# Performance work log

Measured on AMD Instinct MI355X. Metric: run time of the kernel, lower is better.

The kernel has to match this reference:

```python
import jax, jax.numpy as jnp
import numpy as np

EPS = 1e-5

def _conv2d(x, w, b, pad):
    y = jax.lax.conv_general_dilated(x, w, (1, 1), [(pad, pad), (pad, pad)],
                                     dimension_numbers=('NCHW', 'OIHW', 'NCHW'))
    return y + b[None, :, None, None]

def _layernorm2d(x, g, beta):
    # channel-wise LayerNorm per spatial location (LayerNorm2d)
    mu = jnp.mean(x, axis=1, keepdims=True)
    var = jnp.var(x, axis=1, keepdims=True)
    return (x - mu) * jax.lax.rsqrt(var + EPS) * g[None, :, None, None] + beta[None, :, None, None]

def _deform_conv2d(x, offset, w, b, pad):
    # torchvision deform_conv2d semantics (stride 1, dilation 1, 1 group, no mask)
    # x: [B,C,H,W]; offset: [B,2*K*K,H,W] with (dy,dx) per kernel tap; w: [O,C,K,K]
    B, C, H, W = x.shape
    K = w.shape[-1]
    off = offset.reshape(B, K * K, 2, H, W)
    by = jnp.arange(H, dtype=x.dtype)[:, None]   # [H,1]
    bx = jnp.arange(W, dtype=x.dtype)[None, :]   # [1,W]

    def sample(im, py, px):
        # im [C,H,W], py/px [H,W] -> bilinear sample with zero padding outside
        y0 = jnp.floor(py); x0 = jnp.floor(px)
        wy = py - y0; wx = px - x0
        y0i = y0.astype(jnp.int32); x0i = x0.astype(jnp.int32)
        def g(yi, xi):
            valid = (yi >= 0) & (yi < H) & (xi >= 0) & (xi < W)
            v = im[:, jnp.clip(yi, 0, H - 1), jnp.clip(xi, 0, W - 1)]
            return v * valid.astype(im.dtype)
        v00 = g(y0i, x0i);     v01 = g(y0i, x0i + 1)
        v10 = g(y0i + 1, x0i); v11 = g(y0i + 1, x0i + 1)
        return (v00 * (1 - wy) * (1 - wx) + v01 * (1 - wy) * wx
                + v10 * wy * (1 - wx) + v11 * wy * wx)

    vsample = jax.vmap(sample)
    out = jnp.zeros((B, w.shape[0], H, W), dtype=x.dtype)
    for k in range(K * K):  # small fixed tap loop (<=49)
        ki, kj = k // K, k % K
        py = by + (ki - pad) + off[:, k, 0]  # [B,H,W]
        px = bx + (kj - pad) + off[:, k, 1]
        s = vsample(x, py, px)               # [B,C,H,W]
        out = out + jnp.einsum('bchw,oc->bohw', s, w[:, :, ki, kj])
    return out + b[None, :, None, None]


def setup_inputs() -> dict:
    key = jax.random.key(0)
    ks = jax.random.split(key, 12)
    B, C, H, W = 4, 64, 192, 192
    s = 0.02
    inp = {
        'x': jax.random.normal(ks[0], (B, C, H, W), jnp.float32),
        'ln_w': jnp.ones((C,), jnp.float32),
        'ln_b': jnp.zeros((C,), jnp.float32),
        'w_in': jax.random.normal(ks[1], (2 * C, C), jnp.float32) * s,
        'b_in': jnp.zeros((2 * C,), jnp.float32),
        'w_out': jax.random.normal(ks[2], (C, C), jnp.float32) * s,
        'b_out': jnp.zeros((C,), jnp.float32),
        'dw1': jax.random.normal(ks[3], (C, C, 7, 7), jnp.float32) * s,
        'db1': jnp.zeros((C,), jnp.float32),
        'dw2': jax.random.normal(ks[4], (C, C, 5, 5), jnp.float32) * s,
        'db2': jnp.zeros((C,), jnp.float32),
        'dw3': jax.random.normal(ks[5], (C, C, 3, 3), jnp.float32) * s,
        'db3': jnp.zeros((C,), jnp.float32),
        'ow1': jax.random.normal(ks[6], (2 * 7 * 7, C, 5, 5), jnp.float32) * s,
        'ob1': jnp.zeros((2 * 7 * 7,), jnp.float32),
        'ow2': jax.random.normal(ks[7], (2 * 5 * 5, C, 5, 5), jnp.float32) * s,
        'ob2': jnp.zeros((2 * 5 * 5,), jnp.float32),
        'ow3': jax.random.normal(ks[8], (2 * 3 * 3, C, 3, 3), jnp.float32) * s,
        'ob3': jnp.zeros((2 * 3 * 3,), jnp.float32),
    }
    return inp


def reference(x, ln_w, ln_b, w_in, b_in, w_out, b_out,
              dw1, db1, dw2, db2, dw3, db3,
              ow1, ob1, ow2, ob2, ow3, ob3):
    tmp = x
    h = _layernorm2d(x, ln_w, ln_b)
    h = jnp.einsum('bchw,oc->bohw', h, w_in) + b_in[None, :, None, None]  # 1x1 conv_in
    C = x.shape[1]
    x1, x2 = h[:, :C], h[:, C:]
    off = _conv2d(x1, ow1, ob1, 2)
    x1 = _deform_conv2d(x1, off, dw1, db1, 3)
    off = _conv2d(x1, ow2, ob2, 2)
    x1 = _deform_conv2d(x1, off, dw2, db2, 2)
    off = _conv2d(x1, ow3, ob3, 1)
    x1 = _deform_conv2d(x1, off, dw3, db3, 1)
    h = x1 + x2
    h = jnp.einsum('bchw,oc->bohw', h, w_out) + b_out[None, :, None, None]  # 1x1 conv_out
    return h + tmp
```

## Files before the change

kernel.cpp:

```cpp
#include <hip/hip_runtime.h>

#define HH 192
#define WID 192
#define HW (HH*WID)
#define CB 64
#define BB 4
#define NPOS (BB*HW)

typedef __attribute__((ext_vector_type(8))) _Float16 half8v;
typedef __attribute__((ext_vector_type(4))) _Float16 half4v;
typedef __attribute__((ext_vector_type(2))) _Float16 half2v;
typedef __attribute__((ext_vector_type(4))) float f32x4;
typedef __attribute__((ext_vector_type(16))) float f32x16;

static __device__ inline half8v splat8(_Float16 x) {
    half8v v = {x, x, x, x, x, x, x, x};
    return v;
}


template<int KK, int CO, int OP>
__global__ void k_wth(const float* __restrict__ w, _Float16* __restrict__ wt)
{
    int idx = blockIdx.x * 256 + threadIdx.x;
    constexpr int TOT = KK * OP * 64;
    if (idx >= TOT) return;
    int k  = idx / (OP * 64);
    int r  = idx % (OP * 64);
    int cs = r / (OP * 8);
    int r2 = r % (OP * 8);
    int o  = r2 / 8;
    int j  = r2 % 8;
    int c  = cs * 8 + j;
    float v = (o < CO) ? w[((size_t)o * 64 + c) * KK + k] : 0.f;
    wt[idx] = (_Float16)v;
}

__global__ __launch_bounds__(256) void k_lnconv_mfma(
    const float* __restrict__ x, const float* __restrict__ g, const float* __restrict__ be,
    const _Float16* __restrict__ wt_in, const float* __restrict__ b_in,
    _Float16* __restrict__ x1, _Float16* __restrict__ x2)
{
    int p0  = blockIdx.x * 128;
    int b   = p0 / HW;
    int hwb = p0 % HW;

    int lane = threadIdx.x & 63;
    int wave = threadIdx.x >> 6;
    int l31  = lane & 31;
    int h    = lane >> 5;
    int pos  = hwb + wave * 32 + l31;

    const float* xp = x + (size_t)b * CB * HW + pos;

    float v[32];
    float sum = 0.f, sumsq = 0.f;
#pragma unroll
    for (int m = 0; m < 4; m++)
#pragma unroll
        for (int j = 0; j < 8; j++) {
            float t = xp[(size_t)(m * 16 + h * 8 + j) * HW];
            v[m * 8 + j] = t; sum += t; sumsq += t * t;
        }
    sum   += __shfl_xor(sum, 32);
    sumsq += __shfl_xor(sumsq, 32);
    float mu  = sum * (1.f / 64.f);
    float var = sumsq * (1.f / 64.f) - mu * mu;
    float inv = rsqrtf(var + 1e-5f);

    half8v bf[4];
#pragma unroll
    for (int m = 0; m < 4; m++)
#pragma unroll
        for (int j = 0; j < 8; j++) {
            int c = m * 16 + h * 8 + j;
            bf[m][j] = (_Float16)((v[m * 8 + j] - mu) * inv * g[c] + be[c]);
        }

    f32x16 acc[4];
#pragma unroll
    for (int tI = 0; tI < 4; tI++)
#pragma unroll
        for (int r = 0; r < 16; r++) acc[tI][r] = 0.f;

    const half8v* wbase = (const half8v*)wt_in;
#pragma unroll
    for (int m = 0; m < 4; m++) {
        int cs = m * 2 + h;
        const half8v* wp = wbase + (size_t)cs * 128;
#pragma unroll
        for (int tI = 0; tI < 4; tI++) {
            half8v a = wp[tI * 32 + l31];
            acc[tI] = __builtin_amdgcn_mfma_f32_32x32x16_f16(a, bf[m], acc[tI], 0, 0, 0);
        }
    }

    _Float16* o1 = x1 + (size_t)b * HW * 64 + (size_t)pos * 8;
    _Float16* o2 = x2 + (size_t)b * HW * 64 + (size_t)pos * 8;
#pragma unroll
    for (int tI = 0; tI < 4; tI++) {
        _Float16* ob = (tI < 2) ? o1 : o2;
        int obase = (tI & 1) * 32;
#pragma unroll
        for (int gidx = 0; gidx < 4; gidx++) {
            int o = obase + gidx * 8 + 4 * h;
            float4 bb = *(const float4*)&b_in[tI * 32 + gidx * 8 + 4 * h];
            half4v r;
            r[0] = (_Float16)(acc[tI][gidx * 4 + 0] + bb.x);
            r[1] = (_Float16)(acc[tI][gidx * 4 + 1] + bb.y);
            r[2] = (_Float16)(acc[tI][gidx * 4 + 2] + bb.z);
            r[3] = (_Float16)(acc[tI][gidx * 4 + 3] + bb.w);
            *(half4v*)&ob[(size_t)(o >> 3) * HW * 8 + (o & 7)] = r;
        }
    }
}

template<int KD, int PAD, int HALO, int KO, int PADO, int CT>
__global__ __launch_bounds__(256) void k_fconv(
    const _Float16* __restrict__ xin,
    const _Float16* __restrict__ wto, const float* __restrict__ obias,
    const _Float16* __restrict__ wtd, const float* __restrict__ dbias,
    _Float16* __restrict__ outp)
{
    constexpr int KKD = KD * KD;
    constexpr int KKO = KO * KO;
    constexpr int RB = 16 + 2 * HALO;
    constexpr int WB = 8  + 2 * HALO;
    constexpr int OP = CT * 32;

    __shared__ half8v sm[RB * WB * 8];
    __shared__ unsigned int offs[KKD * 128];

    int bi  = blockIdx.x;
    int b   = bi / 288;
    int tt  = bi % 288;
    int by0 = (tt / 24) * 16;
    int bx0 = (tt % 24) * 8;
    int ry0 = by0 - HALO;
    int rx0 = bx0 - HALO;

    const _Float16* xb = xin + (size_t)b * HW * 64;

    {
        _Float16* smlin = (_Float16*)sm;
        constexpr int CH = RB * WB * 8;
        for (int i0 = 0; i0 < CH; i0 += 256) {
            int i    = i0 + (int)threadIdx.x;
            int wbse = i0 + ((int)threadIdx.x & 192);
            if (i < CH) {
                int pix = i >> 3;
                int ts  = i & 7;
                int pl  = ts ^ (pix & 7);
                int r   = pix / WB;
                int cc  = pix - r * WB;
                int yr  = ry0 + r;
                int xc  = rx0 + cc;
                bool ok = (yr >= 0 && yr < HH && xc >= 0 && xc < WID);
                if (ok) {
                    const _Float16* src = xb + ((size_t)pl * HW + (size_t)(yr * WID + xc)) * 8;
                    __builtin_amdgcn_global_load_lds(src, &smlin[(size_t)wbse * 8], 16, 0, 0);
                } else {
                    *(half8v*)&smlin[(size_t)i * 8] = splat8((_Float16)0.f);
                }
            }
        }
    }
    __syncthreads();

    int lane = threadIdx.x & 63;
    int wave = threadIdx.x >> 6;
    int l31  = lane & 31;
    int h    = lane >> 5;
    int prow = l31 >> 3;
    int pcol = l31 & 7;
    int xt   = bx0 + pcol;

    {
        int ct = wave % CT;
        int pp = wave / CT;

        int ytA[CT], pA[CT];
#pragma unroll
        for (int q = 0; q < CT; q++) {
            int g = pp * CT + q;
            ytA[q] = by0 + g * 4 + prow;
            pA[q]  = g * 32 + l31;
        }

        const half8v* wbase = (const half8v*)wto;

        f32x16 accO[CT];
#pragma unroll
        for (int q = 0; q < CT; q++)
#pragma unroll
            for (int r = 0; r < 16; r++) accO[q][r] = 0.f;

        int ki = 0, kj = 0;
        for (int k = 0; k < KKO; k++) {
            int ccx = (xt + kj - PADO) - rx0;
            int pixA[CT];
#pragma unroll
            for (int q = 0; q < CT; q++)
                pixA[q] = ((ytA[q] + ki - PADO) - ry0) * WB + ccx;

#pragma unroll
            for (int m = 0; m < 4; m++) {
                int cs = m * 2 + h;
                const half8v* wp = wbase + ((size_t)k * 8 + cs) * OP;
                half8v a = wp[ct * 32 + l31];
#pragma unroll
                for (int q = 0; q < CT; q++) {
                    half8v bf = sm[pixA[q] * 8 + (cs ^ (pixA[q] & 7))];
                    accO[q] = __builtin_amdgcn_mfma_f32_32x32x16_f16(a, bf, accO[q], 0, 0, 0);
                }
            }

            kj++;
            if (kj == KO) { kj = 0; ki++; }
        }

#pragma unroll
        for (int q = 0; q < CT; q++) {
#pragma unroll
            for (int gi = 0; gi < 4; gi++) {
                int obase = ct * 32 + 8 * gi + 4 * h;
#pragma unroll
                for (int pr = 0; pr < 2; pr++) {
                    int o  = obase + 2 * pr;
                    int kt = o >> 1;
                    if (kt < KKD) {
                        half2v hv;
                        hv[0] = (_Float16)(accO[q][gi * 4 + 2 * pr]     + obias[o]);
                        hv[1] = (_Float16)(accO[q][gi * 4 + 2 * pr + 1] + obias[o + 1]);
                        *(half2v*)&offs[kt * 128 + pA[q]] = hv;
                    }
                }
            }
        }
    }
    __syncthreads();

    int yt   = by0 + wave * 4 + prow;
    int p128 = wave * 32 + l31;

    const half8v* wbase = (const half8v*)wtd;

    f32x16 acc0 = {0.f,0.f,0.f,0.f,0.f,0.f,0.f,0.f,0.f,0.f,0.f,0.f,0.f,0.f,0.f,0.f};
    f32x16 acc1 = {0.f,0.f,0.f,0.f,0.f,0.f,0.f,0.f,0.f,0.f,0.f,0.f,0.f,0.f,0.f,0.f};

    int ki = 0, kj = 0;
    for (int k = 0; k < KKD; k++) {
        half2v ov = *(const half2v*)&offs[k * 128 + p128];
        float ox = (float)ov[0];
        float oy = (float)ov[1];

        half8v a0[4], a1[4];
#pragma unroll
        for (int m = 0; m < 4; m++) {
            int cs = m * 2 + h;
            const half8v* wp = wbase + ((size_t)k * 8 + cs) * 64;
            a0[m] = wp[l31];
            a1[m] = wp[32 + l31];
        }

        float py = (float)(yt + ki - PAD) + ox;
        float px = (float)(xt + kj - PAD) + oy;
        float fy = floorf(py), fx = floorf(px);
        float wy = py - fy, wx = px - fx;
        int iy0 = (int)fy, ix0 = (int)fx;
        int iy1 = iy0 + 1, ix1 = ix0 + 1;
        float m00 = (iy0 >= 0 && iy0 < HH && ix0 >= 0 && ix0 < WID) ? 1.f : 0.f;
        float m01 = (iy0 >= 0 && iy0 < HH && ix1 >= 0 && ix1 < WID) ? 1.f : 0.f;
        float m10 = (iy1 >= 0 && iy1 < HH && ix0 >= 0 && ix0 < WID) ? 1.f : 0.f;
        float m11 = (iy1 >= 0 && iy1 < HH && ix1 >= 0 && ix1 < WID) ? 1.f : 0.f;
        half8v w00v = splat8((_Float16)((1.f - wy) * (1.f - wx) * m00));
        half8v w01v = splat8((_Float16)((1.f - wy) * wx * m01));
        half8v w10v = splat8((_Float16)(wy * (1.f - wx) * m10));
        half8v w11v = splat8((_Float16)(wy * wx * m11));

        bool fast = (iy0 >= ry0) && (iy1 <= ry0 + RB - 1) &&
                    (ix0 >= rx0) && (ix1 <= rx0 + WB - 1);

        if (__builtin_expect(fast, 1)) {
            int p00 = (iy0 - ry0) * WB + (ix0 - rx0);
            int p01 = p00 + 1, p10 = p00 + WB, p11 = p00 + WB + 1;
            int s00 = p00 & 7, s01 = p01 & 7, s10 = p10 & 7, s11 = p11 & 7;
#pragma unroll
            for (int m = 0; m < 4; m++) {
                int cs = m * 2 + h;
                half8v c00 = sm[p00 * 8 + (cs ^ s00)];
                half8v c01 = sm[p01 * 8 + (cs ^ s01)];
                half8v c10 = sm[p10 * 8 + (cs ^ s10)];
                half8v c11 = sm[p11 * 8 + (cs ^ s11)];
                half8v bf = c00 * w00v + c01 * w01v + c10 * w10v + c11 * w11v;
                acc0 = __builtin_amdgcn_mfma_f32_32x32x16_f16(a0[m], bf, acc0, 0, 0, 0);
                acc1 = __builtin_amdgcn_mfma_f32_32x32x16_f16(a1[m], bf, acc1, 0, 0, 0);
            }
        } else {
            int cy0 = min(max(iy0, 0), HH - 1), cy1 = min(max(iy1, 0), HH - 1);
            int cx0 = min(max(ix0, 0), WID - 1), cx1 = min(max(ix1, 0), WID - 1);
            size_t i00 = (size_t)(cy0 * WID + cx0) * 8, i01 = (size_t)(cy0 * WID + cx1) * 8;
            size_t i10 = (size_t)(cy1 * WID + cx0) * 8, i11 = (size_t)(cy1 * WID + cx1) * 8;
#pragma unroll
            for (int m = 0; m < 4; m++) {
                const _Float16* xq = xb + (size_t)(m * 2 + h) * HW * 8;
                half8v c00 = *(const half8v*)(xq + i00);
                half8v c01 = *(const half8v*)(xq + i01);
                half8v c10 = *(const half8v*)(xq + i10);
                half8v c11 = *(const half8v*)(xq + i11);
                half8v bf = c00 * w00v + c01 * w01v + c10 * w10v + c11 * w11v;
                acc0 = __builtin_amdgcn_mfma_f32_32x32x16_f16(a0[m], bf, acc0, 0, 0, 0);
                acc1 = __builtin_amdgcn_mfma_f32_32x32x16_f16(a1[m], bf, acc1, 0, 0, 0);
            }
        }

        kj++;
        if (kj == KD) { kj = 0; ki++; }
    }

    int hwp = yt * WID + xt;
    _Float16* ob = outp + (size_t)b * HW * 64 + (size_t)hwp * 8 + 4 * h;
#pragma unroll
    for (int g = 0; g < 4; g++) {
        float4 bb0 = *(const float4*)&dbias[g * 8 + 4 * h];
        half4v r0;
        r0[0] = (_Float16)(acc0[g * 4 + 0] + bb0.x);
        r0[1] = (_Float16)(acc0[g * 4 + 1] + bb0.y);
        r0[2] = (_Float16)(acc0[g * 4 + 2] + bb0.z);
        r0[3] = (_Float16)(acc0[g * 4 + 3] + bb0.w);
        *(half4v*)&ob[(size_t)g * HW * 8] = r0;
        float4 bb1 = *(const float4*)&dbias[32 + g * 8 + 4 * h];
        half4v r1;
        r1[0] = (_Float16)(acc1[g * 4 + 0] + bb1.x);
        r1[1] = (_Float16)(acc1[g * 4 + 1] + bb1.y);
        r1[2] = (_Float16)(acc1[g * 4 + 2] + bb1.z);
        r1[3] = (_Float16)(acc1[g * 4 + 3] + bb1.w);
        *(half4v*)&ob[(size_t)(4 + g) * HW * 8] = r1;
    }
}

__global__ __launch_bounds__(256) void k_merge_mfma(
    const _Float16* __restrict__ x1f, const _Float16* __restrict__ x2,
    const float* __restrict__ xin, const _Float16* __restrict__ wt_out,
    const float* __restrict__ b_out, float* __restrict__ out)
{
    int p0  = blockIdx.x * 128;
    int b   = p0 / HW;
    int hwb = p0 % HW;

    int lane = threadIdx.x & 63;
    int wave = threadIdx.x >> 6;
    int l31  = lane & 31;
    int h    = lane >> 5;
    int pos  = hwb + wave * 32 + l31;

    const _Float16* a1 = x1f + (size_t)b * HW * 64 + (size_t)pos * 8;
    const _Float16* a2 = x2  + (size_t)b * HW * 64 + (size_t)pos * 8;

    half8v bf[4];
#pragma unroll
    for (int m = 0; m < 4; m++) {
        int cs = m * 2 + h;
        half8v u1 = *(const half8v*)&a1[(size_t)cs * HW * 8];
        half8v u2 = *(const half8v*)&a2[(size_t)cs * HW * 8];
        bf[m] = u1 + u2;
    }

    f32x16 acc[2];
#pragma unroll
    for (int tI = 0; tI < 2; tI++)
#pragma unroll
        for (int r = 0; r < 16; r++) acc[tI][r] = 0.f;

    const half8v* wbase = (const half8v*)wt_out;
#pragma unroll
    for (int m = 0; m < 4; m++) {
        int cs = m * 2 + h;
        const half8v* wp = wbase + (size_t)cs * 64;
#pragma unroll
        for (int tI = 0; tI < 2; tI++) {
            half8v a = wp[tI * 32 + l31];
            acc[tI] = __builtin_amdgcn_mfma_f32_32x32x16_f16(a, bf[m], acc[tI], 0, 0, 0);
        }
    }

    size_t base = (size_t)b * CB * HW + pos;
#pragma unroll
    for (int tI = 0; tI < 2; tI++) {
#pragma unroll
        for (int gidx = 0; gidx < 4; gidx++) {
            int o0 = tI * 32 + gidx * 8 + 4 * h;
#pragma unroll
            for (int i = 0; i < 4; i++) {
                int o = o0 + i;
                out[base + (size_t)o * HW] =
                    acc[tI][gidx * 4 + i] + b_out[o] + xin[base + (size_t)o * HW];
            }
        }
    }
}

extern "C" void kernel_launch(void* const* d_in, const int* in_sizes, int n_in,
                              void* d_out, int out_size, void* d_ws, size_t ws_size,
                              hipStream_t stream)
{
    const float* x     = (const float*)d_in[0];
    const float* ln_w  = (const float*)d_in[1];
    const float* ln_b  = (const float*)d_in[2];
    const float* w_in  = (const float*)d_in[3];
    const float* b_in  = (const float*)d_in[4];
    const float* w_out = (const float*)d_in[5];
    const float* b_out = (const float*)d_in[6];
    const float* dw1   = (const float*)d_in[7];
    const float* db1   = (const float*)d_in[8];
    const float* dw2   = (const float*)d_in[9];
    const float* db2   = (const float*)d_in[10];
    const float* dw3   = (const float*)d_in[11];
    const float* db3   = (const float*)d_in[12];
    const float* ow1   = (const float*)d_in[13];
    const float* ob1   = (const float*)d_in[14];
    const float* ow2   = (const float*)d_in[15];
    const float* ob2   = (const float*)d_in[16];
    const float* ow3   = (const float*)d_in[17];
    const float* ob3   = (const float*)d_in[18];

    _Float16* x1a = (_Float16*)d_ws;
    _Float16* x1b = x1a + (size_t)NPOS * 64;
    _Float16* x2  = x1b + (size_t)NPOS * 64;
    float* off = (float*)(x2 + (size_t)NPOS * 64);
    _Float16* wtd1 = (_Float16*)(off + (size_t)NPOS * 100);
    _Float16* wtd2 = wtd1 + 49 * 64 * 64;
    _Float16* wtd3 = wtd2 + 25 * 64 * 64;
    _Float16* wto1 = wtd3 +  9 * 64 * 64;
    _Float16* wto2 = wto1 + 25 * 128 * 64;
    _Float16* wto3 = wto2 + 25 * 64 * 64;
    _Float16* wtin = wto3 +  9 * 32 * 64;
    _Float16* wtou = wtin + 128 * 64;

    k_wth<49, 64,  64><<<784, 256, 0, stream>>>(dw1, wtd1);
    k_wth<25, 64,  64><<<400, 256, 0, stream>>>(dw2, wtd2);
    k_wth< 9, 64,  64><<<144, 256, 0, stream>>>(dw3, wtd3);
    k_wth<25, 98, 128><<<800, 256, 0, stream>>>(ow1, wto1);
    k_wth<25, 50,  64><<<400, 256, 0, stream>>>(ow2, wto2);
    k_wth< 9, 18,  32><<< 72, 256, 0, stream>>>(ow3, wto3);
    k_wth< 1, 128, 128><<<32, 256, 0, stream>>>(w_in, wtin);
    k_wth< 1, 64,  64><<<16, 256, 0, stream>>>(w_out, wtou);

    k_lnconv_mfma<<<NPOS / 128, 256, 0, stream>>>(x, ln_w, ln_b, wtin, b_in, x1a, x2);

    k_fconv<7, 3, 4, 5, 2, 4><<<1152, 256, 0, stream>>>(x1a, wto1, ob1, wtd1, db1, x1b);
    k_fconv<5, 2, 3, 5, 2, 2><<<1152, 256, 0, stream>>>(x1b, wto2, ob2, wtd2, db2, x1a);
    k_fconv<3, 1, 2, 3, 1, 1><<<1152, 256, 0, stream>>>(x1a, wto3, ob3, wtd3, db3, x1b);

    k_merge_mfma<<<NPOS / 128, 256, 0, stream>>>(x1b, x2, x, wtou, b_out, (float*)d_out);
}
```

Before: 489.1 us.

## Split deformable tap loop across two wave groups with shared-memory reduction

Doubles the fused offset+deform conv blocks from 256 to 512 threads. In the offset-conv phase the extra waves take fewer pixel groups each. In the deform phase the tap range is split in half between two wave groups, and their partial accumulators are summed through shared memory before the output is written. The aim is more parallelism and latency hiding in the gather-heavy sampling loop. The cost is an extra reduction pass and barriers, plus register pressure under the 512-thread launch bound, which may reduce occupancy.

Measured after the change: 483.2 us. About the same (-1.2%).

```diff
diff --git a/kernel.cpp b/kernel.cpp
--- a/kernel.cpp
+++ b/kernel.cpp
@@ -116,7 +116,7 @@
 }
 
 template<int KD, int PAD, int HALO, int KO, int PADO, int CT>
-__global__ __launch_bounds__(256) void k_fconv(
+__global__ __launch_bounds__(512) void k_fconv(
     const _Float16* __restrict__ xin,
     const _Float16* __restrict__ wto, const float* __restrict__ obias,
     const _Float16* __restrict__ wtd, const float* __restrict__ dbias,
@@ -127,6 +127,8 @@
     constexpr int RB = 16 + 2 * HALO;
     constexpr int WB = 8  + 2 * HALO;
     constexpr int OP = CT * 32;
+    constexpr int IPW = (CT * 4 + 7) / 8;
+    constexpr int THALF = (KKD + 1) / 2;
 
     __shared__ half8v sm[RB * WB * 8];
     __shared__ unsigned int offs[KKD * 128];
@@ -144,9 +146,9 @@
     {
         _Float16* smlin = (_Float16*)sm;
         constexpr int CH = RB * WB * 8;
-        for (int i0 = 0; i0 < CH; i0 += 256) {
+        for (int i0 = 0; i0 < CH; i0 += 512) {
             int i    = i0 + (int)threadIdx.x;
-            int wbse = i0 + ((int)threadIdx.x & 192);
+            int wbse = i0 + ((int)threadIdx.x & 448);
             if (i < CH) {
                 int pix = i >> 3;
                 int ts  = i & 7;
@@ -176,31 +178,34 @@
     int xt   = bx0 + pcol;
 
     {
-        int ct = wave % CT;
-        int pp = wave / CT;
-
-        int ytA[CT], pA[CT];
-#pragma unroll
-        for (int q = 0; q < CT; q++) {
-            int g = pp * CT + q;
-            ytA[q] = by0 + g * 4 + prow;
-            pA[q]  = g * 32 + l31;
+        int ct    = wave % CT;
+        int pslot = wave / CT;
+
+        int ytA[IPW], pA[IPW];
+        bool gok[IPW];
+#pragma unroll
+        for (int q = 0; q < IPW; q++) {
+            int g = pslot * IPW + q;
+            gok[q] = (g < 4);
+            int gc = gok[q] ? g : 0;
+            ytA[q] = by0 + gc * 4 + prow;
+            pA[q]  = gc * 32 + l31;
         }
 
         const half8v* wbase = (const half8v*)wto;
 
-        f32x16 accO[CT];
-#pragma unroll
-        for (int q = 0; q < CT; q++)
+        f32x16 accO[IPW];
+#pragma unroll
+        for (int q = 0; q < IPW; q++)
 #pragma unroll
             for (int r = 0; r < 16; r++) accO[q][r] = 0.f;
 
         int ki = 0, kj = 0;
         for (int k = 0; k < KKO; k++) {
             int ccx = (xt + kj - PADO) - rx0;
-            int pixA[CT];
-#pragma unroll
-            for (int q = 0; q < CT; q++)
+            int pixA[IPW];
+#pragma unroll
+            for (int q = 0; q < IPW; q++)
                 pixA[q] = ((ytA[q] + ki - PADO) - ry0) * WB + ccx;
 
 #pragma unroll
@@ -209,7 +214,7 @@
                 const half8v* wp = wbase + ((size_t)k * 8 + cs) * OP;
                 half8v a = wp[ct * 32 + l31];
 #pragma unroll
-                for (int q = 0; q < CT; q++) {
+                for (int q = 0; q < IPW; q++) {
                     half8v bf = sm[pixA[q] * 8 + (cs ^ (pixA[q] & 7))];
                     accO[q] = __builtin_amdgcn_mfma_f32_32x32x16_f16(a, bf, accO[q], 0, 0, 0);
                 }
@@ -220,19 +225,21 @@
         }
 
 #pragma unroll
-        for (int q = 0; q < CT; q++) {
-#pragma unroll
-            for (int gi = 0; gi < 4; gi++) {
-                int obase = ct * 32 + 8 * gi + 4 * h;
-#pragma unroll
-                for (int pr = 0; pr < 2; pr++) {
-                    int o  = obase + 2 * pr;
-                    int kt = o >> 1;
-                    if (kt < KKD) {
-                        half2v hv;
-                        hv[0] = (_Float16)(accO[q][gi * 4 + 2 * pr]     + obias[o]);
-                        hv[1] = (_Float16)(accO[q][gi * 4 + 2 * pr + 1] + obias[o + 1]);
-                        *(half2v*)&offs[kt * 128 + pA[q]] = hv;
+        for (int q = 0; q < IPW; q++) {
+            if (gok[q]) {
+#pragma unroll
+                for (int gi = 0; gi < 4; gi++) {
+                    int obase = ct * 32 + 8 * gi + 4 * h;
+#pragma unroll
+                    for (int pr = 0; pr < 2; pr++) {
+                        int o  = obase + 2 * pr;
+                        int kt = o >> 1;
+                        if (kt < KKD) {
+                            half2v hv;
+                            hv[0] = (_Float16)(accO[q][gi * 4 + 2 * pr]     + obias[o]);
+                            hv[1] = (_Float16)(accO[q][gi * 4 + 2 * pr + 1] + obias[o + 1]);
+                            *(half2v*)&offs[kt * 128 + pA[q]] = hv;
+                        }
                     }
                 }
             }
@@ -240,16 +247,20 @@
     }
     __syncthreads();
 
-    int yt   = by0 + wave * 4 + prow;
-    int p128 = wave * 32 + l31;
+    int w4   = wave & 3;
+    int grp  = wave >> 2;
+    int yt   = by0 + w4 * 4 + prow;
+    int p128 = w4 * 32 + l31;
 
     const half8v* wbase = (const half8v*)wtd;
 
     f32x16 acc0 = {0.f,0.f,0.f,0.f,0.f,0.f,0.f,0.f,0.f,0.f,0.f,0.f,0.f,0.f,0.f,0.f};
     f32x16 acc1 = {0.f,0.f,0.f,0.f,0.f,0.f,0.f,0.f,0.f,0.f,0.f,0.f,0.f,0.f,0.f,0.f};
 
-    int ki = 0, kj = 0;
-    for (int k = 0; k < KKD; k++) {
+    int T0 = grp ? THALF : 0;
+    int T1 = grp ? KKD : THALF;
+    int ki = T0 / KD, kj = T0 % KD;
+    for (int k = T0; k < T1; k++) {
         half2v ov = *(const half2v*)&offs[k * 128 + p128];
         float ox = (float)ov[0];
         float oy = (float)ov[1];
@@ -318,24 +329,38 @@
         if (kj == KD) { kj = 0; ki++; }
     }
 
-    int hwp = yt * WID + xt;
-    _Float16* ob = outp + (size_t)b * HW * 64 + (size_t)hwp * 8 + 4 * h;
-#pragma unroll
-    for (int g = 0; g < 4; g++) {
-        float4 bb0 = *(const float4*)&dbias[g * 8 + 4 * h];
-        half4v r0;
-        r0[0] = (_Float16)(acc0[g * 4 + 0] + bb0.x);
-        r0[1] = (_Float16)(acc0[g * 4 + 1] + bb0.y);
-        r0[2] = (_Float16)(acc0[g * 4 + 2] + bb0.z);
-        r0[3] = (_Float16)(acc0[g * 4 + 3] + bb0.w);
-        *(half4v*)&ob[(size_t)g * HW * 8] = r0;
-        float4 bb1 = *(const float4*)&dbias[32 + g * 8 + 4 * h];
-        half4v r1;
-        r1[0] = (_Float16)(acc1[g * 4 + 0] + bb1.x);
-        r1[1] = (_Float16)(acc1[g * 4 + 1] + bb1.y);
-        r1[2] = (_Float16)(acc1[g * 4 + 2] + bb1.z);
-        r1[3] = (_Float16)(acc1[g * 4 + 3] + bb1.w);
-        *(half4v*)&ob[(size_t)(4 + g) * HW * 8] = r1;
+    __syncthreads();
+    float* red = (float*)sm;
+    if (grp == 1) {
+        float* dst = red + ((size_t)(w4 * 64 + lane)) * 32;
+#pragma unroll
+        for (int r = 0; r < 16; r++) { dst[r] = acc0[r]; dst[16 + r] = acc1[r]; }
+    }
+    __syncthreads();
+    if (grp == 0) {
+        const float* src = red + ((size_t)(w4 * 64 + lane)) * 32;
+#pragma unroll
+        for (int r = 0; r < 16; r++) { acc0[r] += src[r]; acc1[r] += src[16 + r]; }
+
+        int hwp = yt * WID + xt;
+        _Float16* ob = outp + (size_t)b * HW * 64 + (size_t)hwp * 8 + 4 * h;
+#pragma unroll
+        for (int g = 0; g < 4; g++) {
+            float4 bb0 = *(const float4*)&dbias[g * 8 + 4 * h];
+            half4v r0;
+            r0[0] = (_Float16)(acc0[g * 4 + 0] + bb0.x);
+            r0[1] = (_Float16)(acc0[g * 4 + 1] + bb0.y);
+            r0[2] = (_Float16)(acc0[g * 4 + 2] + bb0.z);
+            r0[3] = (_Float16)(acc0[g * 4 + 3] + bb0.w);
+            *(half4v*)&ob[(size_t)g * HW * 8] = r0;
+            float4 bb1 = *(const float4*)&dbias[32 + g * 8 + 4 * h];
+            half4v r1;
+            r1[0] = (_Float16)(acc1[g * 4 + 0] + bb1.x);
+            r1[1] = (_Float16)(acc1[g * 4 + 1] + bb1.y);
+            r1[2] = (_Float16)(acc1[g * 4 + 2] + bb1.z);
+            r1[3] = (_Float16)(acc1[g * 4 + 3] + bb1.w);
+            *(half4v*)&ob[(size_t)(4 + g) * HW * 8] = r1;
+        }
     }
 }
 
@@ -448,9 +473,9 @@
 
     k_lnconv_mfma<<<NPOS / 128, 256, 0, stream>>>(x, ln_w, ln_b, wtin, b_in, x1a, x2);
 
-    k_fconv<7, 3, 4, 5, 2, 4><<<1152, 256, 0, stream>>>(x1a, wto1, ob1, wtd1, db1, x1b);
-    k_fconv<5, 2, 3, 5, 2, 2><<<1152, 256, 0, stream>>>(x1b, wto2, ob2, wtd2, db2, x1a);
-    k_fconv<3, 1, 2, 3, 1, 1><<<1152, 256, 0, stream>>>(x1a, wto3, ob3, wtd3, db3, x1b);
+    k_fconv<7, 3, 4, 5, 2, 4><<<1152, 512, 0, stream>>>(x1a, wto1, ob1, wtd1, db1, x1b);
+    k_fconv<5, 2, 3, 5, 2, 2><<<1152, 512, 0, stream>>>(x1b, wto2, ob2, wtd2, db2, x1a);
+    k_fconv<3, 1, 2, 3, 1, 1><<<1152, 512, 0, stream>>>(x1a, wto3, ob3, wtd3, db3, x1b);
 
     k_merge_mfma<<<NPOS / 128, 256, 0, stream>>>(x1b, x2, x, wtou, b_out, (float*)d_out);
 }
```
